# Kernel optimization log

Hardware: AMD Instinct MI355X
Metric: run time of the kernel (lower is better)

Reference implementation:

```python
import jax, jax.numpy as jnp
import numpy as np
from jax import lax

B, T, I, H = 64, 512, 128, 512
ALPHA = 0.1  # dt/tau = 10/100


def setup_inputs() -> dict:
    key = jax.random.key(0)
    k1, k2, k3 = jax.random.split(key, 3)
    return {
        "x": jax.random.normal(k1, (B, T, I), dtype=jnp.float32),
        "init_state": jnp.zeros((B, H), dtype=jnp.float32),
        "W_in": jax.random.normal(k2, (H, I), dtype=jnp.float32) / np.sqrt(I),
        "b_in": jnp.zeros((H,), dtype=jnp.float32),
        "W_hid": jax.random.normal(k3, (H, H), dtype=jnp.float32) / np.sqrt(H),
        "b_hid": jnp.zeros((H,), dtype=jnp.float32),
        "alpha": jnp.full((H,), ALPHA, dtype=jnp.float32),
    }


def reference(x, init_state, W_in, b_in, W_hid, b_hid, alpha):
    # x: [B, T, I] -> outputs: ([B, T, H], [B, T, H])
    fr0 = jax.nn.relu(init_state)

    def step(carry, u_t):
        fr, v = carry                       # [B, H] each
        v_in = u_t @ W_in.T + b_in          # input Linear
        v_hid = fr @ W_hid.T + b_hid        # hidden Linear
        v_new = (1.0 - alpha) * v + alpha * (v_hid + v_in)   # leaky integration
        v_r = (1.0 - alpha) * v_new + alpha * v_hid          # relaxed state
        fr_new = jax.nn.relu(v_new)
        fr_r = jax.nn.relu(v_r)
        return (fr_new, v_new), (fr_new, fr_r)

    xs = jnp.swapaxes(x, 0, 1)  # [T, B, I]
    _, (states, relax_states) = lax.scan(step, (fr0, init_state), xs)
    return jnp.swapaxes(states, 0, 1), jnp.swapaxes(relax_states, 0, 1)
```

## Files before the change

### kernel.cpp

```cpp
#include <hip/hip_runtime.h>
#include <hip/hip_fp16.h>

#define B_ 64
#define T_ 512
#define I_ 128
#define H_ 512

typedef _Float16 half2v __attribute__((ext_vector_type(2)));
typedef _Float16 f16x8  __attribute__((ext_vector_type(8)));
typedef float    f32x4  __attribute__((ext_vector_type(4)));

__device__ __forceinline__ float dot2(unsigned a, unsigned b, float c) {
    return __builtin_amdgcn_fdot2(__builtin_bit_cast(half2v, a),
                                  __builtin_bit_cast(half2v, b), c, false);
}

__device__ __forceinline__ unsigned short f32_to_f16b(float f) {
    _Float16 h = (_Float16)f;
    return __builtin_bit_cast(unsigned short, h);
}

#define MFMA(ACC, A, Bq) \
    ACC = __builtin_amdgcn_mfma_f32_16x16x32_f16((A), (Bq), (ACC), 0, 0, 0)

__global__ void wconv(const float* __restrict__ Whid,
                      unsigned* __restrict__ Wz) {
    int p = blockIdx.x * 256 + threadIdx.x;
    int m  = p & 3;
    int u4 = p >> 2;
    int l  = u4 & 63;
    int nt = (u4 >> 6) & 3;
    int kt = (u4 >> 8) & 15;
    int w  = (u4 >> 12) & 7;
    int h  = 64 * w + 16 * nt + (l & 15);
    int k  = 32 * kt + 8 * (l >> 4) + 2 * m;
    float w0 = Whid[h * H_ + k];
    float w1 = Whid[h * H_ + k + 1];
    half2v hw = { (_Float16)w0, (_Float16)w1 };
    Wz[p] = __builtin_bit_cast(unsigned, hw);
}

__global__ __launch_bounds__(256) void vin_gemm(const float* __restrict__ x,
                                                const float* __restrict__ Win,
                                                const float* __restrict__ bin,
                                                float* __restrict__ vin) {
    __shared__ __align__(16) unsigned xs[64 * 64];
    __shared__ __align__(16) unsigned ws[64 * 64];
    const int tid = threadIdx.x;
    const int m0 = blockIdx.x * 64;
    const int n0 = blockIdx.y * 64;

    #pragma unroll
    for (int r = 0; r < 8; ++r) {
        int gi = r * 256 + tid;
        int row = gi >> 5;
        int c4 = gi & 31;
        float4 vx = ((const float4*)(x + (size_t)(m0 + row) * I_))[c4];
        float4 vw = ((const float4*)(Win + (size_t)(n0 + row) * I_))[c4];
        int sw = (row >> 2) & 15;
        int col = 4 * ((c4 >> 1) ^ sw) + (c4 & 1) * 2;
        half2v x01 = { (_Float16)vx.x, (_Float16)vx.y };
        half2v x23 = { (_Float16)vx.z, (_Float16)vx.w };
        half2v w01 = { (_Float16)vw.x, (_Float16)vw.y };
        half2v w23 = { (_Float16)vw.z, (_Float16)vw.w };
        xs[row * 64 + col]     = __builtin_bit_cast(unsigned, x01);
        xs[row * 64 + col + 1] = __builtin_bit_cast(unsigned, x23);
        ws[row * 64 + col]     = __builtin_bit_cast(unsigned, w01);
        ws[row * 64 + col + 1] = __builtin_bit_cast(unsigned, w23);
    }
    __syncthreads();

    const int ty = tid >> 4, tx = tid & 15;
    float acc[4][4] = {};
    #pragma unroll
    for (int kb = 0; kb < 16; ++kb) {
        uint4 a4[4], b4[4];
        #pragma unroll
        for (int i = 0; i < 4; ++i)
            a4[i] = *(const uint4*)&xs[(ty * 4 + i) * 64 + 4 * (kb ^ ty)];
        #pragma unroll
        for (int j = 0; j < 4; ++j)
            b4[j] = *(const uint4*)&ws[(tx * 4 + j) * 64 + 4 * (kb ^ tx)];
        #pragma unroll
        for (int i = 0; i < 4; ++i)
            #pragma unroll
            for (int j = 0; j < 4; ++j) {
                acc[i][j] = dot2(a4[i].x, b4[j].x, acc[i][j]);
                acc[i][j] = dot2(a4[i].y, b4[j].y, acc[i][j]);
                acc[i][j] = dot2(a4[i].z, b4[j].z, acc[i][j]);
                acc[i][j] = dot2(a4[i].w, b4[j].w, acc[i][j]);
            }
    }

    float4 bv = ((const float4*)(bin + n0))[tx];
    #pragma unroll
    for (int i = 0; i < 4; ++i) {
        int m = m0 + ty * 4 + i;
        float4 o;
        o.x = acc[i][0] + bv.x; o.y = acc[i][1] + bv.y;
        o.z = acc[i][2] + bv.z; o.w = acc[i][3] + bv.w;
        ((float4*)(vin + (size_t)m * H_ + n0))[tx] = o;
    }
}

__global__ __launch_bounds__(512, 2)
__attribute__((amdgpu_waves_per_eu(2, 2)))
void recurrent(
        const uint4* __restrict__ Wz4,
        const float* __restrict__ vin,
        const float* __restrict__ init_state,
        const float* __restrict__ b_hid,
        const float* __restrict__ alpha,
        float* __restrict__ out0,
        float* __restrict__ out1) {
    __shared__ uint4 ldsWb[8192];
    __shared__ unsigned short fr16[2][512];

    const int t = threadIdx.x;
    const int b = blockIdx.x;
    const int w = t >> 6, l = t & 63;
    const int hi = l >> 4;

    const uint4* wbase = Wz4 + (size_t)w * 4096 + l;

    f16x8 wb[10][4];
    #pragma unroll
    for (int kt = 0; kt < 10; ++kt)
        #pragma unroll
        for (int nt = 0; nt < 4; ++nt) {
            uint4 u = wbase[(kt * 4 + nt) * 64];
            wb[kt][nt] = __builtin_bit_cast(f16x8, u);
            asm("" : "+a"(wb[kt][nt]));
        }

    #pragma unroll
    for (int i = 0; i < 16; ++i)
        ldsWb[w * 1024 + i * 64 + l] = wbase[2560 + i * 64];

    const uint4* gp = wbase + 3584;

    float v = init_state[b * H_ + t];
    fr16[0][t] = f32_to_f16b(fmaxf(v, 0.0f));
    const float bh = b_hid[t];
    const float al = alpha[t];
    const float om = 1.0f - al;
    const bool sel4 = (l & 16) != 0;
    const bool sel5 = (l & 32) != 0;

    const float* vinp = vin + (size_t)b * T_ * H_ + t;
    float* o0 = out0 + (size_t)b * T_ * H_ + t;
    float* o1 = out1 + (size_t)b * T_ * H_ + t;

    __syncthreads();

    for (int s = 0; s < T_; ++s) {
        const int par = s & 1;

        asm volatile("" : "+v"(gp));
        uint4 g0 = gp[0],   g1 = gp[64],  g2 = gp[128], g3 = gp[192];
        uint4 g4 = gp[256], g5 = gp[320], g6 = gp[384], g7 = gp[448];
        float vinv = vinp[(size_t)s * H_];

        f32x4 acc0 = {0.f, 0.f, 0.f, 0.f}, acc1 = {0.f, 0.f, 0.f, 0.f};
        f32x4 acc2 = {0.f, 0.f, 0.f, 0.f}, acc3 = {0.f, 0.f, 0.f, 0.f};

        const f16x8* frb =
            (const f16x8*)((const char*)&fr16[par][0] + hi * 16);

        #pragma unroll
        for (int kt = 0; kt < 10; ++kt) {
            f16x8 afr = frb[kt * 4];
            MFMA(acc0, afr, wb[kt][0]);
            MFMA(acc1, afr, wb[kt][1]);
            MFMA(acc2, afr, wb[kt][2]);
            MFMA(acc3, afr, wb[kt][3]);
        }
        #pragma unroll
        for (int kt = 10; kt < 14; ++kt) {
            f16x8 afr = frb[kt * 4];
            const f16x8* lb =
                (const f16x8*)&ldsWb[w * 1024 + (kt - 10) * 256 + l];
            MFMA(acc0, afr, lb[0]);
            MFMA(acc1, afr, lb[64]);
            MFMA(acc2, afr, lb[128]);
            MFMA(acc3, afr, lb[192]);
        }
        {
            f16x8 a14 = frb[14 * 4];
            MFMA(acc0, a14, __builtin_bit_cast(f16x8, g0));
            MFMA(acc1, a14, __builtin_bit_cast(f16x8, g1));
            MFMA(acc2, a14, __builtin_bit_cast(f16x8, g2));
            MFMA(acc3, a14, __builtin_bit_cast(f16x8, g3));
            f16x8 a15 = frb[15 * 4];
            MFMA(acc0, a15, __builtin_bit_cast(f16x8, g4));
            MFMA(acc1, a15, __builtin_bit_cast(f16x8, g5));
            MFMA(acc2, a15, __builtin_bit_cast(f16x8, g6));
            MFMA(acc3, a15, __builtin_bit_cast(f16x8, g7));
        }

        float s01 = sel4 ? acc1.x : acc0.x;
        float s23 = sel4 ? acc3.x : acc2.x;
        float vh  = sel5 ? s23 : s01;

        float vhid = vh + bh;
        float vnew = om * v + al * (vhid + vinv);
        float frn  = fmaxf(vnew, 0.0f);
        fr16[par ^ 1][t] = f32_to_f16b(frn);
        float vr = om * vnew + al * vhid;
        v = vnew;
        float frr = fmaxf(vr, 0.0f);
        o0[(size_t)s * H_] = frn;
        o1[(size_t)s * H_] = frr;

        asm volatile("s_waitcnt lgkmcnt(0)" ::: "memory");
        __builtin_amdgcn_s_barrier();
    }
}

extern "C" void kernel_launch(void* const* d_in, const int* in_sizes, int n_in,
                              void* d_out, int out_size, void* d_ws, size_t ws_size,
                              hipStream_t stream) {
    const float* x          = (const float*)d_in[0];
    const float* init_state = (const float*)d_in[1];
    const float* W_in       = (const float*)d_in[2];
    const float* b_in       = (const float*)d_in[3];
    const float* W_hid      = (const float*)d_in[4];
    const float* b_hid      = (const float*)d_in[5];
    const float* alpha      = (const float*)d_in[6];

    float* out0 = (float*)d_out;
    float* out1 = out0 + (size_t)B_ * T_ * H_;

    char* ws = (char*)d_ws;
    float*    vin = (float*)ws;
    unsigned* Wz  = (unsigned*)(ws + 67108864);

    hipLaunchKernelGGL(wconv, dim3(512), dim3(256), 0, stream,
                       W_hid, Wz);
    hipLaunchKernelGGL(vin_gemm, dim3(512, 8), dim3(256), 0, stream,
                       x, W_in, b_in, vin);
    hipLaunchKernelGGL(recurrent, dim3(64), dim3(512), 0, stream,
                       (const uint4*)Wz, vin, init_state, b_hid, alpha,
                       out0, out1);
}
```

Measured before the change: 1.035 ms.

## Stream four weight k-tiles from global per step, halve LDS weight cache

```diff
diff --git a/kernel.cpp b/kernel.cpp
--- a/kernel.cpp
+++ b/kernel.cpp
@@ -22,6 +22,7 @@
 
 #define MFMA(ACC, A, Bq) \
     ACC = __builtin_amdgcn_mfma_f32_16x16x32_f16((A), (Bq), (ACC), 0, 0, 0)
+#define BC(u) __builtin_bit_cast(f16x8, u)
 
 __global__ void wconv(const float* __restrict__ Whid,
                       unsigned* __restrict__ Wz) {
@@ -113,7 +114,7 @@
         const float* __restrict__ alpha,
         float* __restrict__ out0,
         float* __restrict__ out1) {
-    __shared__ uint4 ldsWb[8192];
+    __shared__ uint4 ldsWb[4096];
     __shared__ unsigned short fr16[2][512];
 
     const int t = threadIdx.x;
@@ -134,10 +135,10 @@
         }
 
     #pragma unroll
-    for (int i = 0; i < 16; ++i)
-        ldsWb[w * 1024 + i * 64 + l] = wbase[2560 + i * 64];
-
-    const uint4* gp = wbase + 3584;
+    for (int i = 0; i < 8; ++i)
+        ldsWb[w * 512 + i * 64 + l] = wbase[2560 + i * 64];
+
+    const uint4* gp = wbase;
 
     float v = init_state[b * H_ + t];
     fr16[0][t] = f32_to_f16b(fmaxf(v, 0.0f));
@@ -157,8 +158,8 @@
         const int par = s & 1;
 
         asm volatile("" : "+v"(gp));
-        uint4 g0 = gp[0],   g1 = gp[64],  g2 = gp[128], g3 = gp[192];
-        uint4 g4 = gp[256], g5 = gp[320], g6 = gp[384], g7 = gp[448];
+        uint4 gA0 = gp[3072], gA1 = gp[3136], gA2 = gp[3200], gA3 = gp[3264];
+        uint4 gB0 = gp[3328], gB1 = gp[3392], gB2 = gp[3456], gB3 = gp[3520];
         float vinv = vinp[(size_t)s * H_];
 
         f32x4 acc0 = {0.f, 0.f, 0.f, 0.f}, acc1 = {0.f, 0.f, 0.f, 0.f};
@@ -175,27 +176,49 @@
             MFMA(acc2, afr, wb[kt][2]);
             MFMA(acc3, afr, wb[kt][3]);
         }
-        #pragma unroll
-        for (int kt = 10; kt < 14; ++kt) {
-            f16x8 afr = frb[kt * 4];
-            const f16x8* lb =
-                (const f16x8*)&ldsWb[w * 1024 + (kt - 10) * 256 + l];
-            MFMA(acc0, afr, lb[0]);
-            MFMA(acc1, afr, lb[64]);
-            MFMA(acc2, afr, lb[128]);
-            MFMA(acc3, afr, lb[192]);
+        {
+            f16x8 a12 = frb[12 * 4];
+            MFMA(acc0, a12, BC(gA0));
+            MFMA(acc1, a12, BC(gA1));
+            MFMA(acc2, a12, BC(gA2));
+            MFMA(acc3, a12, BC(gA3));
+        }
+        gA0 = gp[3584]; gA1 = gp[3648]; gA2 = gp[3712]; gA3 = gp[3776];
+        {
+            f16x8 a10 = frb[10 * 4];
+            const f16x8* lb = (const f16x8*)&ldsWb[w * 512 + l];
+            MFMA(acc0, a10, lb[0]);
+            MFMA(acc1, a10, lb[64]);
+            MFMA(acc2, a10, lb[128]);
+            MFMA(acc3, a10, lb[192]);
+        }
+        {
+            f16x8 a13 = frb[13 * 4];
+            MFMA(acc0, a13, BC(gB0));
+            MFMA(acc1, a13, BC(gB1));
+            MFMA(acc2, a13, BC(gB2));
+            MFMA(acc3, a13, BC(gB3));
+        }
+        gB0 = gp[3840]; gB1 = gp[3904]; gB2 = gp[3968]; gB3 = gp[4032];
+        {
+            f16x8 a11 = frb[11 * 4];
+            const f16x8* lb = (const f16x8*)&ldsWb[w * 512 + 256 + l];
+            MFMA(acc0, a11, lb[0]);
+            MFMA(acc1, a11, lb[64]);
+            MFMA(acc2, a11, lb[128]);
+            MFMA(acc3, a11, lb[192]);
         }
         {
             f16x8 a14 = frb[14 * 4];
-            MFMA(acc0, a14, __builtin_bit_cast(f16x8, g0));
-            MFMA(acc1, a14, __builtin_bit_cast(f16x8, g1));
-            MFMA(acc2, a14, __builtin_bit_cast(f16x8, g2));
-            MFMA(acc3, a14, __builtin_bit_cast(f16x8, g3));
+            MFMA(acc0, a14, BC(gA0));
+            MFMA(acc1, a14, BC(gA1));
+            MFMA(acc2, a14, BC(gA2));
+            MFMA(acc3, a14, BC(gA3));
             f16x8 a15 = frb[15 * 4];
-            MFMA(acc0, a15, __builtin_bit_cast(f16x8, g4));
-            MFMA(acc1, a15, __builtin_bit_cast(f16x8, g5));
-            MFMA(acc2, a15, __builtin_bit_cast(f16x8, g6));
-            MFMA(acc3, a15, __builtin_bit_cast(f16x8, g7));
+            MFMA(acc0, a15, BC(gB0));
+            MFMA(acc1, a15, BC(gB1));
+            MFMA(acc2, a15, BC(gB2));
+            MFMA(acc3, a15, BC(gB3));
         }
 
         float s01 = sel4 ? acc1.x : acc0.x;
```

Result: slower. 1.238 ms (+19.7%).
